# Performance work log

Measured on AMD Instinct MI355X. Metric: run time of the kernel, lower is better.

Reference implementation:

```python
import jax, jax.numpy as jnp
import numpy as np

KEEP_FRAC = 0.8
HOP_CLIP = 15000  # reached hops are tiny; clip so score fits int32


def _bfs_keep_mask(src, dst, perm, n_nodes):
    """Replicates do_augmentation: BFS hop via u_add_e/min message passing,
    with a tie-break that seeds one unreached node when the frontier stalls,
    then keeps the 80% closest nodes (ties broken by perm)."""
    root = perm[0]
    w = jnp.where(src == dst, 0.0, 1.0).astype(jnp.float32)  # self-loop weight 0
    hop0 = jnp.full((n_nodes,), float(n_nodes), jnp.float32).at[root].set(0.0)
    thresh = n_nodes - 0.5
    cnt_target = int(n_nodes * KEEP_FRAC)

    def cond(state):
        return state[1] <= cnt_target

    def body(state):
        hop, cnt, hc = state
        m = jax.ops.segment_min(hop[src] + w, dst, num_segments=n_nodes)
        hop = jnp.minimum(m, hop)  # min-reduce (self-loops keep hop monotone)
        hc = hc + 1
        new_cnt = jnp.sum(hop < thresh).astype(jnp.int32)
        stuck = new_cnt == cnt
        # pick an unreached node (random in original; perm-ordered here)
        idx = jnp.argmin(jnp.where(hop > thresh, perm, 2 * n_nodes))
        hop = jnp.where(stuck, hop.at[idx].set(hc.astype(jnp.float32)), hop)
        new_cnt = new_cnt + stuck.astype(jnp.int32)
        return hop, new_cnt, hc

    cnt0 = jnp.sum(hop0 < thresh).astype(jnp.int32)
    hop, _, _ = jax.lax.while_loop(cond, body, (hop0, cnt0, jnp.int32(0)))
    score = jnp.minimum(hop, HOP_CLIP).astype(jnp.int32) * n_nodes + perm
    order = jnp.argsort(score)
    keep = jnp.zeros((n_nodes,), bool).at[order[:cnt_target]].set(True)
    return keep


def _gcn(x, src, dst, edge_mask, W_enc, n_nodes):
    # mean-aggregation GCN layer: h = relu(mean_{in-nbrs} x @ W)
    msg = x[src] * edge_mask[:, None]                      # [E, D]
    agg = jax.ops.segment_sum(msg, dst, num_segments=n_nodes)
    deg = jax.ops.segment_sum(edge_mask, dst, num_segments=n_nodes)
    return jax.nn.relu((agg / jnp.maximum(deg, 1.0)[:, None]) @ W_enc)


def _bce_with_logits(logits, positive):
    # BCEWithLogitsLoss: target=1 -> softplus(-x); target=0 -> softplus(x)
    return jnp.mean(jax.nn.softplus(jnp.where(positive, -logits, logits)))


def reference(feat, W_enc, W_disc, src, dst, perm_neg, perm1, perm2):
    n = feat.shape[0]
    ones_e = jnp.ones(src.shape[0], jnp.float32)
    pos = _gcn(feat, src, dst, ones_e, W_enc, n)           # [N, H]
    neg = _gcn(feat[perm_neg], src, dst, ones_e, W_enc, n)

    k = int(n * KEEP_FRAC)
    total = jnp.float32(0.0)
    for perm in (perm1, perm2):
        keep = _bfs_keep_mask(src, dst, perm, n)
        em = (keep[src] & keep[dst]).astype(jnp.float32)
        h = _gcn(feat * keep[:, None], src, dst, em, W_enc, n)
        summary = jax.nn.sigmoid(jnp.sum(h * keep[:, None], axis=0) / k)
        v = W_disc @ summary                               # [H]
        total = total + _bce_with_logits(pos @ v, True) + _bce_with_logits(neg @ v, False)
    return total


def setup_inputs() -> dict:
    key = jax.random.key(0)
    ks = jax.random.split(key, 8)
    N, D, H, DEG = 100000, 64, 64, 16
    E = N * DEG
    src = jnp.concatenate([jax.random.randint(ks[0], (E,), 0, N, jnp.int32),
                           jnp.arange(N, dtype=jnp.int32)])  # + self-loops
    dst = jnp.concatenate([jax.random.randint(ks[1], (E,), 0, N, jnp.int32),
                           jnp.arange(N, dtype=jnp.int32)])
    feat = jax.random.normal(ks[2], (N, D), jnp.float32)
    W_enc = jax.random.normal(ks[3], (D, H), jnp.float32) * (1.0 / np.sqrt(D))
    bound = 1.0 / np.sqrt(H)
    W_disc = jax.random.uniform(ks[4], (H, H), jnp.float32, -bound, bound)
    perm_neg = jax.random.permutation(ks[5], N).astype(jnp.int32)
    perm1 = jax.random.permutation(ks[6], N).astype(jnp.int32)
    perm2 = jax.random.permutation(ks[7], N).astype(jnp.int32)
    return {"feat": feat, "W_enc": W_enc, "W_disc": W_disc, "src": src,
            "dst": dst, "perm_neg": perm_neg, "perm1": perm1, "perm2": perm2}
```

## Files before the change

### kernel.cpp

```cpp
#include <hip/hip_runtime.h>
#include <hip/hip_fp8.h>
#include <hip/hip_fp16.h>

#define BS 256
#define MAXIT 7
#define UNREACHED 0x3f3f3f3f
#define NR 256
#define RB 256

#define C_DONE  0
#define C_CNT   1
#define C_BLKA  2
#define C_BLKB  3
#define C_BLKC  4
#define C_NEWA  20
#define C_LOSS  32
#define C_V1    192
#define C_V2    256

typedef __hip_fp8_e4m3 fp8;

#define ALr(p)   __hip_atomic_load((p), __ATOMIC_RELAXED, __HIP_MEMORY_SCOPE_AGENT)
#define ALf(p)   __hip_atomic_load((p), __ATOMIC_RELAXED, __HIP_MEMORY_SCOPE_AGENT)
#define ASr(p,v) __hip_atomic_store((p),(v), __ATOMIC_RELAXED, __HIP_MEMORY_SCOPE_AGENT)
#define ASl(p,v) __hip_atomic_store((p),(v), __ATOMIC_RELEASE, __HIP_MEMORY_SCOPE_AGENT)

__device__ inline float softplusf(float x){
  return fmaxf(x, 0.f) + log1pf(expf(-fabsf(x)));
}

__device__ inline void cut_hr(const int* __restrict__ ctrl, int target, int& hstar, int& r){
  int c=1;
  hstar=63; r=0;
  for(int h=1;h<=MAXIT;h++){
    int x=ctrl[C_NEWA+h-1];
    if(c+x>target){ hstar=h; r=target-c; return; }
    c+=x;
  }
  r=target-c;
}

__global__ void k_rhist(const int* __restrict__ dst, int E, int* __restrict__ hist, int nbk){
  __shared__ int lh[512];
  int b=blockIdx.x, t=threadIdx.x;
  for(int i=t;i<nbk;i+=BS) lh[i]=0;
  __syncthreads();
  int per=(E+RB-1)/RB;
  int s0=b*per, s1=min(s0+per,E);
  for(int i=s0+t;i<s1;i+=BS) atomicAdd(&lh[dst[i]>>8],1);
  __syncthreads();
  for(int i=t;i<nbk;i+=BS) hist[i*RB+b]=lh[i];
}

__global__ void k_bucketscan(const int* __restrict__ hist, int nbk,
                             int* __restrict__ bktBase, int E){
  __shared__ int tot[512];
  int t=threadIdx.x;
  for(int r=t;r<nbk;r+=BS){
    const int* h=&hist[r*RB];
    int a=0;
    for(int b=0;b<RB;b++) a+=h[b];
    tot[r]=a;
  }
  __syncthreads();
  if(t==0){
    int acc=0;
    for(int r=0;r<nbk;r++){ bktBase[r]=acc; acc+=tot[r]; }
    bktBase[nbk]=E;
  }
}

__global__ void k_rscatter(const int* __restrict__ dst, const int* __restrict__ src, int E,
                           const int* __restrict__ hist, const int* __restrict__ bktBase,
                           unsigned long long* __restrict__ pairs, int nbk){
  __shared__ int cur[512];
  int b=blockIdx.x, t=threadIdx.x;
  for(int r=t;r<nbk;r+=BS){
    int off=bktBase[r];
    const int* h=&hist[r*RB];
    for(int bb=0;bb<b;bb++) off+=h[bb];
    cur[r]=off;
  }
  __syncthreads();
  int per=(E+RB-1)/RB;
  int s0=b*per, s1=min(s0+per,E);
  for(int i=s0+t;i<s1;i+=BS){
    int d=dst[i], s=src[i];
    int pos=atomicAdd(&cur[d>>8],1);
    pairs[pos]=((unsigned long long)(unsigned)d<<32)|(unsigned)s;
  }
}

__global__ void k_bplace2(const int* __restrict__ bktBase, const unsigned long long* __restrict__ pairs,
                          int* __restrict__ rowptr, int* __restrict__ colD, int N, int E){
  __shared__ int cnt[NR];
  __shared__ int s[NR];
  __shared__ int cur[NR];
  int b=blockIdx.x, t=threadIdx.x;
  int v0=b*NR, v1=min(v0+NR,N), nv=v1-v0;
  int s0=bktBase[b], e0=bktBase[b+1];
  cnt[t]=0;
  __syncthreads();
  for(int i=s0+t;i<e0;i+=BS){
    int d=(int)(pairs[i]>>32);
    atomicAdd(&cnt[d-v0],1);
  }
  __syncthreads();
  int v=(t<nv)?cnt[t]:0;
  s[t]=v; __syncthreads();
  for(int o=1;o<BS;o<<=1){
    int x=(t>=o)? s[t-o]:0;
    __syncthreads();
    if(t>=o) s[t]+=x;
    __syncthreads();
  }
  int excl=s[t]-v+s0;
  if(t<nv){ rowptr[v0+t]=excl; cur[t]=excl; }
  if(b==0&&t==0) rowptr[N]=E;
  __syncthreads();
  for(int i=s0+t;i<e0;i+=BS){
    unsigned long long p=pairs[i];
    int d=(int)(p>>32), sv=(int)(p&0xffffffffu);
    int pos=atomicAdd(&cur[d-v0],1);
    colD[pos]=sv;
  }
}

__global__ void k_fw(const float* __restrict__ feat, const float* __restrict__ W,
                     fp8* __restrict__ FWI, int N){
  __shared__ float sW[64*64];
  __shared__ float sf[4][64];
  int t=threadIdx.x;
  for(int i=t;i<64*64;i+=BS) sW[i]=W[i];
  __syncthreads();
  int j=t&63, r=t>>6;
  int ngroups=(N+3)>>2;
  for(int g=blockIdx.x; g<ngroups; g+=gridDim.x){
    int vr=g*4+r;
    sf[r][j] = (vr<N)? feat[vr*64+j] : 0.f;
    __syncthreads();
    if(vr<N){
      float acc=0.f;
      #pragma unroll
      for(int d=0;d<64;d++) acc += sf[r][d]*sW[d*64+j];
      FWI[(size_t)vr*128+j]=fp8(acc);
    }
    __syncthreads();
  }
}

__global__ void k_permrows(unsigned* __restrict__ FWI, const int* __restrict__ pn, int N){
  int i=blockIdx.x*BS+threadIdx.x, st=gridDim.x*BS;
  int tot=N*16;
  for(; i<tot; i+=st){
    int v=i>>4, e=i&15;
    FWI[(size_t)v*32+16+e]=FWI[(size_t)pn[v]*32+e];
  }
}

__global__ void k_bfs_init(int* __restrict__ hop, int N, const int* __restrict__ perm,
                           int* __restrict__ ctrl, unsigned* __restrict__ bits, int nw, int pi){
  int i=blockIdx.x*BS+threadIdx.x, st=gridDim.x*BS;
  int root=perm[0];
  for(int v=i;v<N;v+=st) hop[v]=(v==root)?0:UNREACHED;
  for(int k=i;k<nw;k+=st) bits[k]=0u;
  if(blockIdx.x==0&&threadIdx.x==0){
    ctrl[C_DONE]=0; ctrl[C_CNT]=1;
    ctrl[C_BLKA]=0; ctrl[C_BLKB]=0; ctrl[C_BLKC]=0;
    for(int k=0;k<MAXIT;k++) ctrl[C_NEWA+k]=0;
    if(pi==0) ((float*)ctrl)[C_LOSS]=0.f;
  }
}

__global__ void k_pull(const int* __restrict__ rowptr, const int* __restrict__ col,
                       int* __restrict__ hop, const int* __restrict__ perm,
                       int* __restrict__ ctrl, int it, int N, int target){
  if(ALr(&ctrl[C_DONE])) return;
  int t=threadIdx.x;
  int lvl=it+1;
  int bn=0;
  for(int v=blockIdx.x*BS+t; v<N; v+=gridDim.x*BS){
    if(hop[v]==UNREACHED){
      int b=rowptr[v], e=rowptr[v+1];
      for(int j=b;j<e;j++){
        int s=col[j];
        if(s==v) continue;
        if(hop[s]==lvl-1){ hop[v]=lvl; bn++; break; }
      }
    }
  }
  __shared__ int sred[BS];
  sred[t]=bn; __syncthreads();
  for(int o=BS/2;o>0;o>>=1){ if(t<o) sred[t]+=sred[t+o]; __syncthreads(); }
  __shared__ int isLast, totNew;
  if(t==0){
    if(sred[0]) atomicAdd(&ctrl[C_NEWA+it], sred[0]);
    __threadfence();
    isLast=(atomicAdd(&ctrl[C_BLKA],1)==(int)gridDim.x-1);
  }
  __syncthreads();
  if(!isLast) return;
  __threadfence();
  if(t==0) totNew=ALr(&ctrl[C_NEWA+it]);
  __syncthreads();
  int newly=totNew;
  __shared__ int seeded;
  if(newly==0){
    __shared__ unsigned long long sk[BS];
    unsigned long long key=~0ull;
    for(int v=t; v<N; v+=BS)
      if(ALr(&hop[v])==UNREACHED){
        unsigned long long k=((unsigned long long)(unsigned)perm[v]<<32)|(unsigned)v;
        if(k<key)key=k;
      }
    sk[t]=key; __syncthreads();
    for(int o=BS/2;o>0;o>>=1){ if(t<o&&sk[t+o]<sk[t])sk[t]=sk[t+o]; __syncthreads(); }
    if(t==0){
      seeded=0;
      if(sk[0]!=~0ull){
        int idx=(int)(sk[0]&0xffffffffu);
        ASr(&hop[idx],lvl);
        ctrl[C_NEWA+it]=1;
        seeded=1;
      }
    }
    __syncthreads();
    newly=seeded;
  }
  if(t==0){
    int c=ctrl[C_CNT]+newly;
    ctrl[C_CNT]=c;
    if(c>target) ASl(&ctrl[C_DONE],1);
    ASr(&ctrl[C_BLKA],0);
    __threadfence();
  }
}

__global__ void k_flagscan(const int* __restrict__ hop, const int* __restrict__ perm,
                           unsigned* __restrict__ bits, int* __restrict__ wordpref,
                           int N, int nw, int* __restrict__ ctrl, int target){
  int t=threadIdx.x;
  int hstar,rr; cut_hr(ctrl,target,hstar,rr);
  for(int v=blockIdx.x*BS+t; v<N; v+=gridDim.x*BS)
    if(min(hop[v],63)==hstar){
      int p=perm[v];
      atomicOr(&bits[p>>5], 1u<<(p&31));
    }
  __shared__ int isLast;
  if(t==0){
    __threadfence();
    isLast=(atomicAdd(&ctrl[C_BLKC],1)==(int)gridDim.x-1);
  }
  __syncthreads();
  if(!isLast) return;
  __threadfence();
  __shared__ int ss[BS];
  __shared__ int carry;
  if(t==0) carry=0;
  __syncthreads();
  for(int base=0; base<nw; base+=BS){
    int i=base+t;
    int v=(i<nw)? __popc(ALr(&bits[i])) : 0;
    ss[t]=v; __syncthreads();
    for(int o=1;o<BS;o<<=1){
      int x=(t>=o)? ss[t-o]:0;
      __syncthreads();
      if(t>=o) ss[t]+=x;
      __syncthreads();
    }
    if(i<nw) wordpref[i]=carry+ss[t]-v;
    __syncthreads();
    if(t==0) carry+=ss[BS-1];
    __syncthreads();
  }
  if(t==0){ ASr(&ctrl[C_BLKC],0); __threadfence(); }
}

__global__ void k_keep(const int* __restrict__ hop, const int* __restrict__ perm,
                       const unsigned* __restrict__ bits, const int* __restrict__ wordpref,
                       int* __restrict__ keepPk, int N, const int* __restrict__ ctrl,
                       int pi, int target){
  int hstar,r; cut_hr(ctrl,target,hstar,r);
  int i=blockIdx.x*BS+threadIdx.x, st=gridDim.x*BS;
  for(int v=i;v<N;v+=st){
    int h=min(hop[v],63), kp=0;
    if(h<hstar) kp=1;
    else if(h==hstar){
      int p=perm[v];
      unsigned mask=(2u<<(p&31))-1u;
      int cum=wordpref[p>>5]+__popc(bits[p>>5]&mask);
      kp=(cum<=r);
    }
    if(pi==0) keepPk[v]=kp; else keepPk[v]|=kp<<1;
  }
}

__global__ void __launch_bounds__(BS, 8) k_mega(
    const int* __restrict__ rowptr, const int* __restrict__ col,
    const unsigned char* __restrict__ FWI8, const int* __restrict__ keepPk,
    __half* __restrict__ P, __half* __restrict__ Q,
    float* __restrict__ sp1, float* __restrict__ sp2, int N){
  __shared__ uint4 lds4[4][8][8];
  __shared__ float sh1[4][64], sh2[4][64];
  int t=threadIdx.x, lane=t&63, w=t>>6;
  int eidx=lane>>3, q=lane&7;
  int woff=lane>>2, bsh=(lane&3)*8;
  volatile unsigned* l32=(volatile unsigned*)&lds4[w][0][0];
  int wid=(blockIdx.x*BS+t)>>6, nw=(gridDim.x*BS)>>6;
  float acc1=0.f, acc2=0.f;
  for(int v=wid; v<N; v+=nw){
    int b=rowptr[v], e=rowptr[v+1];
    int deg=e-b;
    int kv=keepPk[v];
    float ap=0.f, an=0.f, a1=0.f, a2=0.f;
    int c1t=0, c2t=0;
    for(int c0=b; c0<e; c0+=8){
      int n=min(8, e-c0);
      uint4 wa=make_uint4(0,0,0,0);
      int kk=0;
      if(eidx<n){
        int s=col[c0+eidx];
        if(q==0) kk=keepPk[s];
        wa=*reinterpret_cast<const uint4*>(FWI8+((size_t)s<<7)+(q<<4));
      }
      lds4[w][eidx][q]=wa;
      __asm__ volatile("" ::: "memory");
      unsigned long long bal1=__ballot(q==0 && (kk&1));
      unsigned long long bal2=__ballot(q==0 && (kk&2));
      c1t+=__popcll(bal1); c2t+=__popcll(bal2);
      if(n==8){
        #pragma unroll
        for(int ee=0; ee<8; ee++){
          unsigned ua=l32[ee*32+woff];
          unsigned ub=l32[ee*32+16+woff];
          fp8 ha, hb;
          ha.__x=(unsigned char)(ua>>bsh);
          hb.__x=(unsigned char)(ub>>bsh);
          float fa=(float)ha, fb=(float)hb;
          ap+=fa; an+=fb;
          a1 += ((bal1>>(ee*8))&1) ? fa : 0.f;
          a2 += ((bal2>>(ee*8))&1) ? fa : 0.f;
        }
      } else {
        for(int ee=0; ee<n; ee++){
          unsigned ua=l32[ee*32+woff];
          unsigned ub=l32[ee*32+16+woff];
          fp8 ha, hb;
          ha.__x=(unsigned char)(ua>>bsh);
          hb.__x=(unsigned char)(ub>>bsh);
          float fa=(float)ha, fb=(float)hb;
          ap+=fa; an+=fb;
          a1 += ((bal1>>(ee*8))&1) ? fa : 0.f;
          a2 += ((bal2>>(ee*8))&1) ? fa : 0.f;
        }
      }
      __asm__ volatile("" ::: "memory");
    }
    float invd=1.f/(float)deg;
    float p =fmaxf(ap*invd, 0.f);
    float qq=fmaxf(an*invd, 0.f);
    P[(size_t)v*64+lane]=__float2half(p);
    Q[(size_t)v*64+lane]=__float2half(qq);
    if(kv&1) acc1+=fmaxf(a1/(float)max(c1t,1), 0.f);
    if(kv&2) acc2+=fmaxf(a2/(float)max(c2t,1), 0.f);
  }
  sh1[w][lane]=acc1; sh2[w][lane]=acc2;
  __syncthreads();
  if(w==0){
    sp1[blockIdx.x*64+lane]=sh1[0][lane]+sh1[1][lane]+sh1[2][lane]+sh1[3][lane];
    sp2[blockIdx.x*64+lane]=sh2[0][lane]+sh2[1][lane]+sh2[2][lane]+sh2[3][lane];
  }
}

__global__ void k_redsum(const float* __restrict__ sp1, const float* __restrict__ sp2,
                         int nb, int rows, float* __restrict__ sp1b, float* __restrict__ sp2b,
                         const float* __restrict__ Wd, float* __restrict__ cf,
                         int* __restrict__ ctrl, float invk){
  __shared__ float s[BS];
  int t=threadIdx.x, lane=t&63, p=t>>6;
  int base=blockIdx.x*rows;
  float a=0.f;
  for(int r=p; r<rows; r+=4){ int row=base+r; if(row<nb) a+=sp1[row*64+lane]; }
  s[t]=a; __syncthreads();
  if(t<64) sp1b[blockIdx.x*64+t]=s[t]+s[t+64]+s[t+128]+s[t+192];
  __syncthreads();
  a=0.f;
  for(int r=p; r<rows; r+=4){ int row=base+r; if(row<nb) a+=sp2[row*64+lane]; }
  s[t]=a; __syncthreads();
  if(t<64) sp2b[blockIdx.x*64+t]=s[t]+s[t+64]+s[t+128]+s[t+192];
  __shared__ int isLast;
  __syncthreads();
  if(t==0){
    __threadfence();
    isLast=(atomicAdd(&ctrl[C_BLKB],1)==(int)gridDim.x-1);
  }
  __syncthreads();
  if(!isLast) return;
  __threadfence();
  int nb2=gridDim.x;
  __shared__ float sig[64];
  a=0.f;
  for(int b=p;b<nb2;b+=4) a+=ALf(&sp1b[b*64+lane]);
  s[t]=a; __syncthreads();
  if(t<64){
    float x=(s[t]+s[t+64]+s[t+128]+s[t+192])*invk;
    sig[t]=1.f/(1.f+expf(-x));
  }
  __syncthreads();
  if(t<64){
    float acc=0.f;
    #pragma unroll
    for(int d=0;d<64;d++) acc+=Wd[t*64+d]*sig[d];
    cf[C_V1+t]=acc;
  }
  __syncthreads();
  a=0.f;
  for(int b=p;b<nb2;b+=4) a+=ALf(&sp2b[b*64+lane]);
  s[t]=a; __syncthreads();
  if(t<64){
    float x=(s[t]+s[t+64]+s[t+128]+s[t+192])*invk;
    sig[t]=1.f/(1.f+expf(-x));
  }
  __syncthreads();
  if(t<64){
    float acc=0.f;
    #pragma unroll
    for(int d=0;d<64;d++) acc+=Wd[t*64+d]*sig[d];
    cf[C_V2+t]=acc;
  }
  if(t==0){ ASr(&ctrl[C_BLKB],0); __threadfence(); }
}

__global__ void k_loss2(const __half* __restrict__ P, const __half* __restrict__ Q,
                        float* __restrict__ cf, int N){
  __shared__ float sv1[64], sv2[64];
  __shared__ float sred[BS];
  int t=threadIdx.x;
  if(t<64){ sv1[t]=cf[C_V1+t]; sv2[t]=cf[C_V2+t]; }
  __syncthreads();
  int i=blockIdx.x*BS+t, st=gridDim.x*BS;
  float acc=0.f;
  for(int v=i; v<N; v+=st){
    const uint4* pr=(const uint4*)(P+(size_t)v*64);
    const uint4* qr=(const uint4*)(Q+(size_t)v*64);
    float a1=0.f,a2=0.f,b1=0.f,b2=0.f;
    #pragma unroll
    for(int c=0;c<8;c++){
      uint4 pu=pr[c], qu=qr[c];
      unsigned arr[4]={pu.x,pu.y,pu.z,pu.w};
      unsigned brr[4]={qu.x,qu.y,qu.z,qu.w};
      #pragma unroll
      for(int j=0;j<4;j++){
        int d=c*8+j*2;
        __half2 ph=*(const __half2*)&arr[j];
        __half2 qh=*(const __half2*)&brr[j];
        float2 pf=__half22float2(ph);
        float2 qf=__half22float2(qh);
        a1=fmaf(pf.x,sv1[d],a1); a1=fmaf(pf.y,sv1[d+1],a1);
        a2=fmaf(pf.x,sv2[d],a2); a2=fmaf(pf.y,sv2[d+1],a2);
        b1=fmaf(qf.x,sv1[d],b1); b1=fmaf(qf.y,sv1[d+1],b1);
        b2=fmaf(qf.x,sv2[d],b2); b2=fmaf(qf.y,sv2[d+1],b2);
      }
    }
    acc += softplusf(-a1)+softplusf(b1)+softplusf(-a2)+softplusf(b2);
  }
  sred[t]=acc;
  __syncthreads();
  for(int o=BS/2;o>0;o>>=1){ if(t<o) sred[t]+=sred[t+o]; __syncthreads(); }
  if(t==0) atomicAdd(&cf[C_LOSS], sred[0]);
}

__global__ void k_final(const float* __restrict__ cf, float* __restrict__ out, int N){
  if(blockIdx.x||threadIdx.x) return;
  out[0]=cf[C_LOSS]/(float)N;
}

extern "C" void kernel_launch(void* const* d_in, const int* in_sizes, int n_in,
                              void* d_out, int out_size, void* d_ws, size_t ws_size,
                              hipStream_t stream) {
  const float* feat    = (const float*)d_in[0];
  const float* Wenc    = (const float*)d_in[1];
  const float* Wdisc   = (const float*)d_in[2];
  const int*   src     = (const int*)d_in[3];
  const int*   dst     = (const int*)d_in[4];
  const int*   permneg = (const int*)d_in[5];
  const int*   perm1   = (const int*)d_in[6];
  const int*   perm2   = (const int*)d_in[7];
  float* out = (float*)d_out;

  int N = in_sizes[5];
  int E = in_sizes[3];
  int target = (int)((double)N*0.8);
  int NB = (N+BS-1)/BS;
  int WORDS = (N+31)/32;
  int NBK = (N+NR-1)/NR;
  const int SUBB = 2048;
  const int R1B = 128, R1ROWS = SUBB/R1B;

  char* w = (char*)d_ws;
  auto alloc = [&](size_t bytes)->void*{
    void* p = (void*)w;
    w += (bytes + 255) & ~(size_t)255;
    return p;
  };
  int*      ctrl    = (int*)     alloc(4096);
  int*      rowptrD = (int*)     alloc((size_t)(N+1)*4);
  int*      histD   = (int*)     alloc((size_t)RB*NBK*4);
  int*      bktBase = (int*)     alloc((size_t)(NBK+1)*4);
  int*      colD    = (int*)     alloc((size_t)E*4);
  unsigned long long* pairs = (unsigned long long*)alloc((size_t)E*8);
  int*      hop     = (int*)     alloc((size_t)N*4);
  int*      keepPk  = (int*)     alloc((size_t)N*4);
  unsigned* bits    = (unsigned*)alloc((size_t)WORDS*4);
  int*      wordpref= (int*)     alloc((size_t)(WORDS+1)*4);
  fp8*      FWI     = (fp8*)     alloc((size_t)N*128);
  __half*   P       = (__half*)  alloc((size_t)N*64*2);
  __half*   Q       = (__half*)  alloc((size_t)N*64*2);
  float*    sp1     = (float*)   alloc((size_t)SUBB*64*4);
  float*    sp2     = (float*)   alloc((size_t)SUBB*64*4);
  float*    sp1b    = (float*)   alloc((size_t)R1B*64*4);
  float*    sp2b    = (float*)   alloc((size_t)R1B*64*4);
  float*    cf = (float*)ctrl;

  k_rhist     <<<RB,  BS, 0, stream>>>(dst, E, histD, NBK);
  k_bucketscan<<<1,   BS, 0, stream>>>(histD, NBK, bktBase, E);
  k_rscatter  <<<RB,  BS, 0, stream>>>(dst, src, E, histD, bktBase, pairs, NBK);
  k_bplace2   <<<NBK, BS, 0, stream>>>(bktBase, pairs, rowptrD, colD, N, E);

  k_fw      <<<2048, BS, 0, stream>>>(feat, Wenc, FWI, N);
  k_permrows<<<4096, BS, 0, stream>>>((unsigned*)FWI, permneg, N);

  const int* perms[2] = {perm1, perm2};
  for(int pi=0; pi<2; pi++){
    const int* perm = perms[pi];
    k_bfs_init<<<NB, BS, 0, stream>>>(hop, N, perm, ctrl, bits, WORDS, pi);
    for(int it=0; it<MAXIT; it++)
      k_pull<<<NB, BS, 0, stream>>>(rowptrD, colD, hop, perm, ctrl, it, N, target);
    k_flagscan<<<NB, BS, 0, stream>>>(hop, perm, bits, wordpref, N, WORDS, ctrl, target);
    k_keep    <<<NB, BS, 0, stream>>>(hop, perm, bits, wordpref, keepPk, N, ctrl, pi, target);
  }

  k_mega  <<<SUBB, BS, 0, stream>>>(rowptrD, colD, (const unsigned char*)FWI, keepPk,
                                    P, Q, sp1, sp2, N);
  k_redsum<<<R1B, BS, 0, stream>>>(sp1, sp2, SUBB, R1ROWS, sp1b, sp2b, Wdisc, cf, ctrl,
                                   1.f/(float)target);

  k_loss2<<<NB, BS, 0, stream>>>(P, Q, cf, N);
  k_final<<<1, 1, 0, stream>>>(cf, out, N);
}
```

Before: 557.3 us.

## Batch both BFS augmentations into shared launches and fold small kernels via last-block

Runs the two BFS mask computations (init, pull iterations, flag scan, keep) for perm1 and perm2 in the same launches by doubling the grid and giving each half its own hop, bits, prefix and control block. The single-block bucket scan is folded into the histogram kernel through a last-block-done pattern, and the per-block cursor prefix in the scatter is precomputed by a new parallel scan kernel. The final loss division moves into the loss kernel's last block. The aim is to halve the serial BFS launch chain, run both BFS passes concurrently for more parallelism, and remove the quadratic cursor loop, at the cost of an extra memset, more workspace and more last-block atomic synchronisation.

```diff
diff --git a/kernel.cpp b/kernel.cpp
--- a/kernel.cpp
+++ b/kernel.cpp
@@ -29,18 +29,19 @@
   return fmaxf(x, 0.f) + log1pf(expf(-fabsf(x)));
 }
 
-__device__ inline void cut_hr(const int* __restrict__ ctrl, int target, int& hstar, int& r){
+__device__ inline void cut_hr(const int* __restrict__ ctl, int target, int& hstar, int& r){
   int c=1;
   hstar=63; r=0;
   for(int h=1;h<=MAXIT;h++){
-    int x=ctrl[C_NEWA+h-1];
+    int x=ctl[C_NEWA+h-1];
     if(c+x>target){ hstar=h; r=target-c; return; }
     c+=x;
   }
   r=target-c;
 }
 
-__global__ void k_rhist(const int* __restrict__ dst, int E, int* __restrict__ hist, int nbk){
+__global__ void k_rhist(const int* __restrict__ dst, int E, int* __restrict__ hist,
+                        int* __restrict__ bktBase, int nbk, int* __restrict__ ctrl){
   __shared__ int lh[512];
   int b=blockIdx.x, t=threadIdx.x;
   for(int i=t;i<nbk;i+=BS) lh[i]=0;
@@ -50,37 +51,53 @@
   for(int i=s0+t;i<s1;i+=BS) atomicAdd(&lh[dst[i]>>8],1);
   __syncthreads();
   for(int i=t;i<nbk;i+=BS) hist[i*RB+b]=lh[i];
-}
-
-__global__ void k_bucketscan(const int* __restrict__ hist, int nbk,
-                             int* __restrict__ bktBase, int E){
-  __shared__ int tot[512];
-  int t=threadIdx.x;
+  __shared__ int isLast;
+  __syncthreads();
+  if(t==0){
+    __threadfence();
+    isLast=(atomicAdd(&ctrl[C_BLKA],1)==(int)gridDim.x-1);
+  }
+  __syncthreads();
+  if(!isLast) return;
+  __threadfence();
   for(int r=t;r<nbk;r+=BS){
     const int* h=&hist[r*RB];
     int a=0;
-    for(int b=0;b<RB;b++) a+=h[b];
-    tot[r]=a;
+    for(int bb=0;bb<RB;bb++) a+=ALr(&h[bb]);
+    lh[r]=a;
   }
   __syncthreads();
   if(t==0){
     int acc=0;
-    for(int r=0;r<nbk;r++){ bktBase[r]=acc; acc+=tot[r]; }
+    for(int r=0;r<nbk;r++){ bktBase[r]=acc; acc+=lh[r]; }
     bktBase[nbk]=E;
-  }
+    ASr(&ctrl[C_BLKA],0);
+    __threadfence();
+  }
+}
+
+__global__ void k_cursors(const int* __restrict__ hist, const int* __restrict__ bktBase,
+                          int* __restrict__ cursorTab, int nbk){
+  __shared__ int s[BS];
+  int r=blockIdx.x, t=threadIdx.x;
+  if(r>=nbk) return;
+  int v=hist[r*RB+t];
+  s[t]=v; __syncthreads();
+  for(int o=1;o<BS;o<<=1){
+    int x=(t>=o)? s[t-o]:0;
+    __syncthreads();
+    if(t>=o) s[t]+=x;
+    __syncthreads();
+  }
+  cursorTab[r*RB+t]=bktBase[r]+s[t]-v;
 }
 
 __global__ void k_rscatter(const int* __restrict__ dst, const int* __restrict__ src, int E,
-                           const int* __restrict__ hist, const int* __restrict__ bktBase,
+                           const int* __restrict__ cursorTab,
                            unsigned long long* __restrict__ pairs, int nbk){
   __shared__ int cur[512];
   int b=blockIdx.x, t=threadIdx.x;
-  for(int r=t;r<nbk;r+=BS){
-    int off=bktBase[r];
-    const int* h=&hist[r*RB];
-    for(int bb=0;bb<b;bb++) off+=h[bb];
-    cur[r]=off;
-  }
+  for(int r=t;r<nbk;r+=BS) cur[r]=cursorTab[r*RB+b];
   __syncthreads();
   int per=(E+RB-1)/RB;
   int s0=b*per, s1=min(s0+per,E);
@@ -158,28 +175,43 @@
   }
 }
 
-__global__ void k_bfs_init(int* __restrict__ hop, int N, const int* __restrict__ perm,
-                           int* __restrict__ ctrl, unsigned* __restrict__ bits, int nw, int pi){
-  int i=blockIdx.x*BS+threadIdx.x, st=gridDim.x*BS;
+__global__ void k_init2(int* __restrict__ hop1, int* __restrict__ hop2, int N,
+                        const int* __restrict__ perm1, const int* __restrict__ perm2,
+                        int* __restrict__ ctrl,
+                        unsigned* __restrict__ bits1, unsigned* __restrict__ bits2,
+                        int nw, int NB){
+  int pb = blockIdx.x>=NB;
+  int lb = blockIdx.x - (pb?NB:0);
+  int* hop = pb? hop2:hop1;
+  const int* perm = pb? perm2:perm1;
+  unsigned* bits = pb? bits2:bits1;
+  int* ctl = ctrl + pb*1024;
+  int i=lb*BS+threadIdx.x, st=NB*BS;
   int root=perm[0];
   for(int v=i;v<N;v+=st) hop[v]=(v==root)?0:UNREACHED;
   for(int k=i;k<nw;k+=st) bits[k]=0u;
-  if(blockIdx.x==0&&threadIdx.x==0){
-    ctrl[C_DONE]=0; ctrl[C_CNT]=1;
-    ctrl[C_BLKA]=0; ctrl[C_BLKB]=0; ctrl[C_BLKC]=0;
-    for(int k=0;k<MAXIT;k++) ctrl[C_NEWA+k]=0;
-    if(pi==0) ((float*)ctrl)[C_LOSS]=0.f;
-  }
-}
-
-__global__ void k_pull(const int* __restrict__ rowptr, const int* __restrict__ col,
-                       int* __restrict__ hop, const int* __restrict__ perm,
-                       int* __restrict__ ctrl, int it, int N, int target){
-  if(ALr(&ctrl[C_DONE])) return;
+  if(lb==0&&threadIdx.x==0){
+    ctl[C_DONE]=0; ctl[C_CNT]=1;
+    ctl[C_BLKA]=0; ctl[C_BLKB]=0; ctl[C_BLKC]=0;
+    for(int k=0;k<MAXIT;k++) ctl[C_NEWA+k]=0;
+    if(!pb) ((float*)ctl)[C_LOSS]=0.f;
+  }
+}
+
+__global__ void k_pull2(const int* __restrict__ rowptr, const int* __restrict__ col,
+                        int* __restrict__ hop1, int* __restrict__ hop2,
+                        const int* __restrict__ perm1, const int* __restrict__ perm2,
+                        int* __restrict__ ctrl, int it, int N, int target, int NB){
+  int pb = blockIdx.x>=NB;
+  int lb = blockIdx.x - (pb?NB:0);
+  int* hop = pb? hop2:hop1;
+  const int* perm = pb? perm2:perm1;
+  int* ctl = ctrl + pb*1024;
+  if(ALr(&ctl[C_DONE])) return;
   int t=threadIdx.x;
   int lvl=it+1;
   int bn=0;
-  for(int v=blockIdx.x*BS+t; v<N; v+=gridDim.x*BS){
+  for(int v=lb*BS+t; v<N; v+=NB*BS){
     if(hop[v]==UNREACHED){
       int b=rowptr[v], e=rowptr[v+1];
       for(int j=b;j<e;j++){
@@ -194,14 +226,14 @@
   for(int o=BS/2;o>0;o>>=1){ if(t<o) sred[t]+=sred[t+o]; __syncthreads(); }
   __shared__ int isLast, totNew;
   if(t==0){
-    if(sred[0]) atomicAdd(&ctrl[C_NEWA+it], sred[0]);
-    __threadfence();
-    isLast=(atomicAdd(&ctrl[C_BLKA],1)==(int)gridDim.x-1);
+    if(sred[0]) atomicAdd(&ctl[C_NEWA+it], sred[0]);
+    __threadfence();
+    isLast=(atomicAdd(&ctl[C_BLKA],1)==NB-1);
   }
   __syncthreads();
   if(!isLast) return;
   __threadfence();
-  if(t==0) totNew=ALr(&ctrl[C_NEWA+it]);
+  if(t==0) totNew=ALr(&ctl[C_NEWA+it]);
   __syncthreads();
   int newly=totNew;
   __shared__ int seeded;
@@ -220,7 +252,7 @@
       if(sk[0]!=~0ull){
         int idx=(int)(sk[0]&0xffffffffu);
         ASr(&hop[idx],lvl);
-        ctrl[C_NEWA+it]=1;
+        ctl[C_NEWA+it]=1;
         seeded=1;
       }
     }
@@ -228,20 +260,29 @@
     newly=seeded;
   }
   if(t==0){
-    int c=ctrl[C_CNT]+newly;
-    ctrl[C_CNT]=c;
-    if(c>target) ASl(&ctrl[C_DONE],1);
-    ASr(&ctrl[C_BLKA],0);
-    __threadfence();
-  }
-}
-
-__global__ void k_flagscan(const int* __restrict__ hop, const int* __restrict__ perm,
-                           unsigned* __restrict__ bits, int* __restrict__ wordpref,
-                           int N, int nw, int* __restrict__ ctrl, int target){
+    int c=ctl[C_CNT]+newly;
+    ctl[C_CNT]=c;
+    if(c>target) ASl(&ctl[C_DONE],1);
+    ASr(&ctl[C_BLKA],0);
+    __threadfence();
+  }
+}
+
+__global__ void k_flagscan2(const int* __restrict__ hop1, const int* __restrict__ hop2,
+                            const int* __restrict__ perm1, const int* __restrict__ perm2,
+                            unsigned* __restrict__ bits1, unsigned* __restrict__ bits2,
+                            int* __restrict__ wordpref1, int* __restrict__ wordpref2,
+                            int N, int nw, int* __restrict__ ctrl, int target, int NB){
+  int pb = blockIdx.x>=NB;
+  int lb = blockIdx.x - (pb?NB:0);
+  const int* hop = pb? hop2:hop1;
+  const int* perm = pb? perm2:perm1;
+  unsigned* bits = pb? bits2:bits1;
+  int* wordpref = pb? wordpref2:wordpref1;
+  int* ctl = ctrl + pb*1024;
   int t=threadIdx.x;
-  int hstar,rr; cut_hr(ctrl,target,hstar,rr);
-  for(int v=blockIdx.x*BS+t; v<N; v+=gridDim.x*BS)
+  int hstar,rr; cut_hr(ctl,target,hstar,rr);
+  for(int v=lb*BS+t; v<N; v+=NB*BS)
     if(min(hop[v],63)==hstar){
       int p=perm[v];
       atomicOr(&bits[p>>5], 1u<<(p&31));
@@ -249,7 +290,7 @@
   __shared__ int isLast;
   if(t==0){
     __threadfence();
-    isLast=(atomicAdd(&ctrl[C_BLKC],1)==(int)gridDim.x-1);
+    isLast=(atomicAdd(&ctl[C_BLKC],1)==NB-1);
   }
   __syncthreads();
   if(!isLast) return;
@@ -273,25 +314,36 @@
     if(t==0) carry+=ss[BS-1];
     __syncthreads();
   }
-  if(t==0){ ASr(&ctrl[C_BLKC],0); __threadfence(); }
-}
-
-__global__ void k_keep(const int* __restrict__ hop, const int* __restrict__ perm,
-                       const unsigned* __restrict__ bits, const int* __restrict__ wordpref,
-                       int* __restrict__ keepPk, int N, const int* __restrict__ ctrl,
-                       int pi, int target){
-  int hstar,r; cut_hr(ctrl,target,hstar,r);
+  if(t==0){ ASr(&ctl[C_BLKC],0); __threadfence(); }
+}
+
+__global__ void k_keep2(const int* __restrict__ hop1, const int* __restrict__ hop2,
+                        const int* __restrict__ perm1, const int* __restrict__ perm2,
+                        const unsigned* __restrict__ bits1, const unsigned* __restrict__ bits2,
+                        const int* __restrict__ wordpref1, const int* __restrict__ wordpref2,
+                        int* __restrict__ keepPk, int N, const int* __restrict__ ctrl, int target){
+  int h1,r1,h2,r2;
+  cut_hr(ctrl,target,h1,r1);
+  cut_hr(ctrl+1024,target,h2,r2);
   int i=blockIdx.x*BS+threadIdx.x, st=gridDim.x*BS;
   for(int v=i;v<N;v+=st){
-    int h=min(hop[v],63), kp=0;
-    if(h<hstar) kp=1;
-    else if(h==hstar){
-      int p=perm[v];
+    int h=min(hop1[v],63), kp1=0;
+    if(h<h1) kp1=1;
+    else if(h==h1){
+      int p=perm1[v];
       unsigned mask=(2u<<(p&31))-1u;
-      int cum=wordpref[p>>5]+__popc(bits[p>>5]&mask);
-      kp=(cum<=r);
-    }
-    if(pi==0) keepPk[v]=kp; else keepPk[v]|=kp<<1;
+      int cum=wordpref1[p>>5]+__popc(bits1[p>>5]&mask);
+      kp1=(cum<=r1);
+    }
+    h=min(hop2[v],63); int kp2=0;
+    if(h<h2) kp2=1;
+    else if(h==h2){
+      int p=perm2[v];
+      unsigned mask=(2u<<(p&31))-1u;
+      int cum=wordpref2[p>>5]+__popc(bits2[p>>5]&mask);
+      kp2=(cum<=r2);
+    }
+    keepPk[v]=kp1|(kp2<<1);
   }
 }
 
@@ -432,7 +484,8 @@
 }
 
 __global__ void k_loss2(const __half* __restrict__ P, const __half* __restrict__ Q,
-                        float* __restrict__ cf, int N){
+                        float* __restrict__ cf, int* __restrict__ ctrl,
+                        float* __restrict__ out, int N){
   __shared__ float sv1[64], sv2[64];
   __shared__ float sred[BS];
   int t=threadIdx.x;
@@ -467,12 +520,18 @@
   sred[t]=acc;
   __syncthreads();
   for(int o=BS/2;o>0;o>>=1){ if(t<o) sred[t]+=sred[t+o]; __syncthreads(); }
-  if(t==0) atomicAdd(&cf[C_LOSS], sred[0]);
-}
-
-__global__ void k_final(const float* __restrict__ cf, float* __restrict__ out, int N){
-  if(blockIdx.x||threadIdx.x) return;
-  out[0]=cf[C_LOSS]/(float)N;
+  __shared__ int isLast;
+  if(t==0){
+    atomicAdd(&cf[C_LOSS], sred[0]);
+    __threadfence();
+    isLast=(atomicAdd(&ctrl[C_BLKC],1)==(int)gridDim.x-1);
+  }
+  __syncthreads();
+  if(t==0 && isLast){
+    __threadfence();
+    out[0]=ALf(&cf[C_LOSS])/(float)N;
+    ASr(&ctrl[C_BLKC],0);
+  }
 }
 
 extern "C" void kernel_launch(void* const* d_in, const int* in_sizes, int n_in,
@@ -503,48 +562,51 @@
     w += (bytes + 255) & ~(size_t)255;
     return p;
   };
-  int*      ctrl    = (int*)     alloc(4096);
-  int*      rowptrD = (int*)     alloc((size_t)(N+1)*4);
-  int*      histD   = (int*)     alloc((size_t)RB*NBK*4);
-  int*      bktBase = (int*)     alloc((size_t)(NBK+1)*4);
-  int*      colD    = (int*)     alloc((size_t)E*4);
+  int*      ctrl     = (int*)     alloc(8192);
+  int*      rowptrD  = (int*)     alloc((size_t)(N+1)*4);
+  int*      histD    = (int*)     alloc((size_t)RB*NBK*4);
+  int*      cursorTab= (int*)     alloc((size_t)RB*NBK*4);
+  int*      bktBase  = (int*)     alloc((size_t)(NBK+1)*4);
+  int*      colD     = (int*)     alloc((size_t)E*4);
   unsigned long long* pairs = (unsigned long long*)alloc((size_t)E*8);
-  int*      hop     = (int*)     alloc((size_t)N*4);
-  int*      keepPk  = (int*)     alloc((size_t)N*4);
-  unsigned* bits    = (unsigned*)alloc((size_t)WORDS*4);
-  int*      wordpref= (int*)     alloc((size_t)(WORDS+1)*4);
-  fp8*      FWI     = (fp8*)     alloc((size_t)N*128);
-  __half*   P       = (__half*)  alloc((size_t)N*64*2);
-  __half*   Q       = (__half*)  alloc((size_t)N*64*2);
-  float*    sp1     = (float*)   alloc((size_t)SUBB*64*4);
-  float*    sp2     = (float*)   alloc((size_t)SUBB*64*4);
-  float*    sp1b    = (float*)   alloc((size_t)R1B*64*4);
-  float*    sp2b    = (float*)   alloc((size_t)R1B*64*4);
+  int*      hop1     = (int*)     alloc((size_t)N*4);
+  int*      hop2     = (int*)     alloc((size_t)N*4);
+  int*      keepPk   = (int*)     alloc((size_t)N*4);
+  unsigned* bits1    = (unsigned*)alloc((size_t)WORDS*4);
+  unsigned* bits2    = (unsigned*)alloc((size_t)WORDS*4);
+  int*      wordpref1= (int*)     alloc((size_t)(WORDS+1)*4);
+  int*      wordpref2= (int*)     alloc((size_t)(WORDS+1)*4);
+  fp8*      FWI      = (fp8*)     alloc((size_t)N*128);
+  __half*   P        = (__half*)  alloc((size_t)N*64*2);
+  __half*   Q        = (__half*)  alloc((size_t)N*64*2);
+  float*    sp1      = (float*)   alloc((size_t)SUBB*64*4);
+  float*    sp2      = (float*)   alloc((size_t)SUBB*64*4);
+  float*    sp1b     = (float*)   alloc((size_t)R1B*64*4);
+  float*    sp2b     = (float*)   alloc((size_t)R1B*64*4);
   float*    cf = (float*)ctrl;
 
-  k_rhist     <<<RB,  BS, 0, stream>>>(dst, E, histD, NBK);
-  k_bucketscan<<<1,   BS, 0, stream>>>(histD, NBK, bktBase, E);
-  k_rscatter  <<<RB,  BS, 0, stream>>>(dst, src, E, histD, bktBase, pairs, NBK);
-  k_bplace2   <<<NBK, BS, 0, stream>>>(bktBase, pairs, rowptrD, colD, N, E);
+  hipMemsetAsync(ctrl, 0, 8192, stream);
+
+  k_rhist   <<<RB,  BS, 0, stream>>>(dst, E, histD, bktBase, NBK, ctrl);
+  k_cursors <<<NBK, BS, 0, stream>>>(histD, bktBase, cursorTab, NBK);
+  k_rscatter<<<RB,  BS, 0, stream>>>(dst, src, E, cursorTab, pairs, NBK);
+  k_bplace2 <<<NBK, BS, 0, stream>>>(bktBase, pairs, rowptrD, colD, N, E);
 
   k_fw      <<<2048, BS, 0, stream>>>(feat, Wenc, FWI, N);
   k_permrows<<<4096, BS, 0, stream>>>((unsigned*)FWI, permneg, N);
 
-  const int* perms[2] = {perm1, perm2};
-  for(int pi=0; pi<2; pi++){
-    const int* perm = perms[pi];
-    k_bfs_init<<<NB, BS, 0, stream>>>(hop, N, perm, ctrl, bits, WORDS, pi);
-    for(int it=0; it<MAXIT; it++)
-      k_pull<<<NB, BS, 0, stream>>>(rowptrD, colD, hop, perm, ctrl, it, N, target);
-    k_flagscan<<<NB, BS, 0, stream>>>(hop, perm, bits, wordpref, N, WORDS, ctrl, target);
-    k_keep    <<<NB, BS, 0, stream>>>(hop, perm, bits, wordpref, keepPk, N, ctrl, pi, target);
-  }
+  k_init2<<<2*NB, BS, 0, stream>>>(hop1, hop2, N, perm1, perm2, ctrl, bits1, bits2, WORDS, NB);
+  for(int it=0; it<MAXIT; it++)
+    k_pull2<<<2*NB, BS, 0, stream>>>(rowptrD, colD, hop1, hop2, perm1, perm2, ctrl, it, N, target, NB);
+  k_flagscan2<<<2*NB, BS, 0, stream>>>(hop1, hop2, perm1, perm2, bits1, bits2,
+                                       wordpref1, wordpref2, N, WORDS, ctrl, target, NB);
+  k_keep2    <<<2*NB, BS, 0, stream>>>(hop1, hop2, perm1, perm2, bits1, bits2,
+                                       wordpref1, wordpref2, keepPk, N, ctrl, target);
 
   k_mega  <<<SUBB, BS, 0, stream>>>(rowptrD, colD, (const unsigned char*)FWI, keepPk,
                                     P, Q, sp1, sp2, N);
   k_redsum<<<R1B, BS, 0, stream>>>(sp1, sp2, SUBB, R1ROWS, sp1b, sp2b, Wdisc, cf, ctrl,
                                    1.f/(float)target);
 
-  k_loss2<<<NB, BS, 0, stream>>>(P, Q, cf, N);
-  k_final<<<1, 1, 0, stream>>>(cf, out, N);
-}
+  k_loss2<<<NB, BS, 0, stream>>>(P, Q, cf, ctrl, out, N);
+}
```

Result: no change. 547.5 us (-1.8%).
